# Kernel optimization log

Hardware: AMD Instinct MI355X
Metric: run time of the kernel (lower is better)

Reference implementation:

```python
import jax, jax.numpy as jnp
import numpy as np

N, D, R, DR, H, L = 6000, 128, 1000, 128, 2, 2
MAXN = 1.0 - 4e-3  # Poincare ball projection boundary (c=1)


def _norm(x):
    return jnp.clip(jnp.linalg.norm(x, axis=-1, keepdims=True), 1e-15)


def proj(x):
    n = _norm(x)
    return jnp.where(n > MAXN, x / n * MAXN, x)


def expmap0(u):
    n = _norm(u)
    return proj(jnp.tanh(n) * u / n)


def logmap0(p):
    n = _norm(p)
    return jnp.arctanh(jnp.minimum(n, 1.0 - 1e-7)) * p / n


def mobius_add(x, y):
    x2 = jnp.sum(x * x, -1, keepdims=True)
    y2 = jnp.sum(y * y, -1, keepdims=True)
    xy = jnp.sum(x * y, -1, keepdims=True)
    num = (1 + 2 * xy + y2) * x + (1 - x2) * y
    den = 1 + 2 * xy + x2 * y2
    return num / jnp.clip(den, 1e-15)


def hgc_layer(x, adj, W, b):
    # HypLinear (mobius matvec + hyperbolic bias), HypAgg (tangent-space SpMM), HypAct (relu)
    mv = proj(expmap0(logmap0(x) @ W.T))
    h = proj(mobius_add(mv, proj(expmap0(b))))
    h = proj(expmap0(adj @ logmap0(h)))
    return proj(expmap0(jax.nn.relu(logmap0(h))))


def gat_layer(x, adj, W, a_src, a_dst):
    h = jnp.einsum('nd,hde->hne', x, W)                 # [H,N,D]
    es = jnp.einsum('hne,he->hn', h, a_src)
    ed = jnp.einsum('hne,he->hn', h, a_dst)
    e = jax.nn.leaky_relu(es[:, :, None] + ed[:, None, :], 0.2)  # [H,N,N]
    att = jax.nn.softmax(jnp.where(adj[None] > 0, e, -1e9), axis=-1)
    out = jnp.einsum('hnm,hme->hne', att, h).mean(0)    # head-average -> [N,D]
    return jax.nn.elu(out)


def mha(x, Wq, Wk, Wv, Wfc, g, b):
    # Transformer-style MHA with residual + LayerNorm; x: [N, Lr, D]
    Nn, Lr, _ = x.shape
    split = lambda y: y.reshape(Nn, Lr, H, D).transpose(0, 2, 1, 3)
    q, k, v = split(x @ Wq), split(x @ Wk), split(x @ Wv)
    attn = jax.nn.softmax(jnp.einsum('nhld,nhmd->nhlm', q, k) / jnp.sqrt(jnp.float32(D)), -1)
    o = jnp.einsum('nhlm,nhmd->nhld', attn, v).transpose(0, 2, 1, 3).reshape(Nn, Lr, H * D)
    o = o @ Wfc + x
    mu = o.mean(-1, keepdims=True)
    var = o.var(-1, keepdims=True)
    return g * (o - mu) / jnp.sqrt(var + 1e-6) + b


def _forward(ent_sr, ent_tg, rel_sr, rel_tg, adj_sr, adj_tg, rel_adj_sr, rel_adj_tg,
             gat_W, gat_a_src, gat_a_dst, Wq, Wk, Wv, Wfc, ln_g, ln_b, hgc_W, hgc_b):
    # Relation Aggregator: sparse mm + rowsum normalization
    def rel_agg(radj, remb):
        return (radj @ remb) / radj.sum(-1, keepdims=True)
    sr_rel = rel_agg(rel_adj_sr, rel_sr)
    tg_rel = rel_agg(rel_adj_tg, rel_tg)

    # Attentive Neighbor Aggregator + multi-range fusion (res=True -> range = L+1)
    def branch(x, adj):
        outs, h = [x], x
        for i in range(L):
            h = gat_layer(h, adj, gat_W[i], gat_a_src[i], gat_a_dst[i])
            h = h / jnp.clip(_norm(h), 1e-12)  # F.normalize(dim=1)
            outs.append(h)
        seq = jnp.stack(outs, axis=1)  # [N, L+1, D]
        return mha(seq, Wq, Wk, Wv, Wfc, ln_g, ln_b).mean(1)
    sr = branch(ent_sr, adj_sr)
    tg = branch(ent_tg, adj_tg)

    # Hyperbolic encoder (proj_tan0 is identity for PoincareBall)
    def encode(x, adj):
        h = expmap0(x)
        for i in range(2):
            h = hgc_layer(h, adj, hgc_W[i], hgc_b[i])
        return logmap0(h)
    hs = ent_sr + encode(ent_sr, adj_sr)
    ht = ent_tg + encode(ent_tg, adj_tg)

    return (jnp.concatenate([sr, sr_rel], -1), jnp.concatenate([tg, tg_rel], -1),
            jnp.concatenate([hs, sr_rel], -1), jnp.concatenate([ht, tg_rel], -1))


def setup_inputs() -> dict:
    key = jax.random.key(0)
    ks = jax.random.split(key, 24)

    def make_adj(k):
        m = jax.random.bernoulli(k, 32.0 / N, (N, N)) | jnp.eye(N, dtype=bool)
        a = m.astype(jnp.float32)
        return a / a.sum(-1, keepdims=True)

    def make_rel_adj(k1, k2):
        m = jax.random.bernoulli(k1, 5.0 / R, (N, R)).astype(jnp.float32)
        idx = jax.random.randint(k2, (N,), 0, R)
        return m.at[jnp.arange(N), idx].set(1.0)  # guarantee positive rowsum

    return {
        'ent_sr': 0.02 * jax.random.normal(ks[0], (N, D)),
        'ent_tg': 0.02 * jax.random.normal(ks[1], (N, D)),
        'rel_sr': 0.02 * jax.random.normal(ks[2], (R, DR)),
        'rel_tg': 0.02 * jax.random.normal(ks[3], (R, DR)),
        'adj_sr': make_adj(ks[4]),
        'adj_tg': make_adj(ks[5]),
        'rel_adj_sr': make_rel_adj(ks[6], ks[7]),
        'rel_adj_tg': make_rel_adj(ks[8], ks[9]),
        'gat_W': 0.1 * jax.random.normal(ks[10], (L, H, D, D)),
        'gat_a_src': 0.1 * jax.random.normal(ks[11], (L, H, D)),
        'gat_a_dst': 0.1 * jax.random.normal(ks[12], (L, H, D)),
        'Wq': 0.05 * jax.random.normal(ks[13], (D, H * D)),
        'Wk': 0.05 * jax.random.normal(ks[14], (D, H * D)),
        'Wv': 0.05 * jax.random.normal(ks[15], (D, H * D)),
        'Wfc': 0.05 * jax.random.normal(ks[16], (H * D, D)),
        'ln_g': jnp.ones((D,)),
        'ln_b': jnp.zeros((D,)),
        'hgc_W': 0.05 * jax.random.normal(ks[17], (2, D, D)),
        'hgc_b': 0.01 * jax.random.normal(ks[18], (2, D)),
    }


def reference(ent_sr, ent_tg, rel_sr, rel_tg, adj_sr, adj_tg, rel_adj_sr, rel_adj_tg,
              gat_W, gat_a_src, gat_a_dst, Wq, Wk, Wv, Wfc, ln_g, ln_b, hgc_W, hgc_b):
    return _forward(ent_sr, ent_tg, rel_sr, rel_tg, adj_sr, adj_tg, rel_adj_sr, rel_adj_tg,
                    gat_W, gat_a_src, gat_a_dst, Wq, Wk, Wv, Wfc, ln_g, ln_b, hgc_W, hgc_b)
```

## Files before the change

### kernel.cpp

```cpp
#include <hip/hip_runtime.h>
#include <hip/hip_bf16.h>
#include <math.h>

#define NN   6000
#define N2   12000
#define DD   128
#define RR   1000
#define CAP  96
#define CAPR 48
#define MAXN_F 0.996f

typedef short  bf16x8 __attribute__((ext_vector_type(8)));
typedef float  f32x4  __attribute__((ext_vector_type(4)));
typedef unsigned u32x4 __attribute__((ext_vector_type(4)));

__device__ int      g_dt[19];
__device__ unsigned g_csri[N2 * CAP];
__device__ int      g_cnt[N2];
__device__ float    g_seq[N2 * 3 * DD];
__device__ unsigned short g_seqb[3 * N2 * DD];
__device__ unsigned short g_hhb[N2 * 256];
__device__ float    g_es[2][N2];
__device__ float    g_ed[2][N2];
__device__ unsigned short g_qkvb[(size_t)N2 * 3 * 768];
__device__ unsigned short g_ob[(size_t)N2 * 3 * 256];
__device__ float    g_fc[N2 * 3 * DD];
__device__ float    g_t[N2 * DD];
__device__ float    g_t2[N2 * DD];
__device__ unsigned short g_WgatT[2][256 * DD];
__device__ unsigned short g_WqkvT[768 * DD];
__device__ unsigned short g_WfcT[DD * 256];
__device__ float    g_WhgcT[2][DD * DD];

__device__ __forceinline__ float ldin(const void* p, size_t i, int bf) {
    if (bf) return __uint_as_float(((unsigned)((const unsigned short*)p)[i]) << 16);
    return ((const float*)p)[i];
}
__device__ __forceinline__ unsigned short f2b(float f) {
    unsigned u = __float_as_uint(f);
    u += 0x7FFFu + ((u >> 16) & 1u);
    return (unsigned short)(u >> 16);
}
__device__ __forceinline__ float b2f(unsigned short b) {
    return __uint_as_float(((unsigned)b) << 16);
}
__device__ __forceinline__ float adjval(int c) {
    return b2f(f2b(1.0f / (float)c));
}

__device__ __forceinline__ float wsum(float v) {
    #pragma unroll
    for (int o = 32; o > 0; o >>= 1) v += __shfl_xor(v, o, 64);
    return v;
}
__device__ __forceinline__ float wmax(float v) {
    #pragma unroll
    for (int o = 32; o > 0; o >>= 1) v = fmaxf(v, __shfl_xor(v, o, 64));
    return v;
}

struct P19 { const void* p[19]; };

__global__ void detect_all(P19 ptrs) {
    const int sizes[19] = {768000,768000,128000,128000,36000000,36000000,6000000,6000000,
                           65536,512,512,32768,32768,32768,32768,128,128,32768,256};
    __shared__ int votes[2];
    if (threadIdx.x == 0) { votes[0] = 0; votes[1] = 0; }
    __syncthreads();
    int slot = blockIdx.x < 19 ? blockIdx.x : 17;
    const unsigned* p = (const unsigned*)ptrs.p[slot];
    int nwords = sizes[slot] / 2;
    if (nwords > 0) {
        int nsamp = nwords < 4096 ? nwords : 4096;
        int stride = nwords / nsamp; if (stride < 1) stride = 1;
        for (int s = threadIdx.x; s < nsamp; s += blockDim.x) {
            unsigned lo = p[(size_t)s * stride] & 0xFFFFu;
            if (lo) {
                unsigned e = (lo >> 7) & 0xFFu;
                if (e >= 100u && e <= 140u) atomicAdd(&votes[1], 1);
                else                        atomicAdd(&votes[0], 1);
            }
        }
    }
    __syncthreads();
    int isbf = (votes[1] > votes[0]) ? 1 : 0;
    if (blockIdx.x < 19) {
        if (threadIdx.x == 0) g_dt[blockIdx.x] = isbf;
    } else {
        for (int i = threadIdx.x; i < 32768; i += blockDim.x) {
            int j = i & 127, d = (i >> 7) & 127, l = i >> 14;
            g_WhgcT[l][j * 128 + d] = ldin(ptrs.p[17], i, isbf);
        }
    }
}

__device__ __forceinline__ void bias_wave(const void* hgc_b, int layer, int lane,
                                          float& y0, float& y1, float& y2) {
    float b0 = ldin(hgc_b, (size_t)layer * DD + lane, g_dt[18]);
    float b1 = ldin(hgc_b, (size_t)layer * DD + 64 + lane, g_dt[18]);
    float ss = wsum(b0 * b0 + b1 * b1);
    float nrm = fmaxf(sqrtf(ss), 1e-15f);
    float t = tanhf(nrm);
    float s = t / nrm;
    float vn = t;
    if (t > MAXN_F) { s *= MAXN_F / t; vn = MAXN_F; }
    y0 = s * b0; y1 = s * b1;
    y2 = vn * vn;
}

__device__ __forceinline__ void hgc_lin_w(const float* uw, int layer, int lane,
                                          float y0, float y1, float y2,
                                          float& o0, float& o1) {
    const float* W = g_WhgcT[layer];
    float mv0 = 0.f, mv1 = 0.f;
    #pragma unroll 16
    for (int j = 0; j < DD; j++) {
        float uj = uw[j];
        mv0 = fmaf(W[j * 128 + lane], uj, mv0);
        mv1 = fmaf(W[j * 128 + 64 + lane], uj, mv1);
    }
    float ss2 = wsum(mv0 * mv0 + mv1 * mv1);
    float nm = fmaxf(sqrtf(ss2), 1e-15f);
    float t2 = tanhf(nm);
    float sc = t2 / nm; float xn = t2;
    if (t2 > MAXN_F) { sc *= MAXN_F / t2; xn = MAXN_F; }
    float x0 = sc * mv0, x1 = sc * mv1;
    float x2 = xn * xn;
    float xy = wsum(x0 * y0 + x1 * y1);
    float a = 1.f + 2.f * xy + y2;
    float den = 1.f + 2.f * xy + x2 * y2;
    den = (fabsf(den) < 1e-15f) ? 1e-15f : den;
    float h0 = (a * x0 + (1.f - x2) * y0) / den;
    float h1 = (a * x1 + (1.f - x2) * y1) / den;
    float s3 = wsum(h0 * h0 + h1 * h1);
    float nn = fmaxf(sqrtf(s3), 1e-15f);
    float f = 1.f;
    if (nn > MAXN_F) { f = MAXN_F / nn; nn = MAXN_F; }
    float lg = atanhf(fminf(nn, 1.f - 1e-7f)) / nn;
    o0 = lg * f * h0; o1 = lg * f * h1;
}

__device__ __forceinline__ void hgc_agg_w(const float* tin, int n, int which, int lane,
                                          unsigned* bas, float& o0, float& o1) {
    int c = min(g_cnt[n], CAP);
    const unsigned* idx = &g_csri[(size_t)n * CAP];
    if (lane < c)      bas[lane]      = (idx[lane]      + (unsigned)(which * NN)) * 128u;
    if (64 + lane < c) bas[64 + lane] = (idx[64 + lane] + (unsigned)(which * NN)) * 128u;
    float a0 = 0.f, a1 = 0.f;
    int j = 0;
    for (; j + 4 <= c; j += 4) {
        unsigned b0 = bas[j], b1 = bas[j + 1], b2 = bas[j + 2], b3 = bas[j + 3];
        float v0 = tin[(size_t)b0 + lane], v1 = tin[(size_t)b1 + lane];
        float v2 = tin[(size_t)b2 + lane], v3 = tin[(size_t)b3 + lane];
        float w0 = tin[(size_t)b0 + 64 + lane], w1 = tin[(size_t)b1 + 64 + lane];
        float w2 = tin[(size_t)b2 + 64 + lane], w3 = tin[(size_t)b3 + 64 + lane];
        a0 += (v0 + v1) + (v2 + v3);
        a1 += (w0 + w1) + (w2 + w3);
    }
    for (; j < c; j++) {
        unsigned bb = bas[j];
        a0 += tin[(size_t)bb + lane];
        a1 += tin[(size_t)bb + 64 + lane];
    }
    float sc = (c > 0) ? adjval(c) : 0.f;
    a0 *= sc; a1 *= sc;
    float ss = wsum(a0 * a0 + a1 * a1);
    float nm = fmaxf(sqrtf(ss), 1e-15f);
    float t = tanhf(nm);
    float s1 = t / nm; float xn = t;
    if (t > MAXN_F) { s1 *= MAXN_F / t; xn = MAXN_F; }
    float lg = atanhf(fminf(xn, 1.f - 1e-7f)) / fmaxf(xn, 1e-15f);
    float u0 = fmaxf(lg * s1 * a0, 0.f), u1 = fmaxf(lg * s1 * a1, 0.f);
    float ss2 = wsum(u0 * u0 + u1 * u1);
    float nm2 = fmaxf(sqrtf(ss2), 1e-15f);
    float t2 = tanhf(nm2);
    float s2 = t2 / nm2; float xn2 = t2;
    if (t2 > MAXN_F) { s2 *= MAXN_F / t2; xn2 = MAXN_F; }
    float lg2 = atanhf(fminf(xn2, 1.f - 1e-7f)) / fmaxf(xn2, 1e-15f);
    o0 = lg2 * s2 * u0; o1 = lg2 * s2 * u1;
}

__global__ __launch_bounds__(256) void front_mega(P19 in, float* __restrict__ out) {
    int b = blockIdx.x;
    int tid = threadIdx.x;
    int w = tid >> 6, lane = tid & 63;
    int phase, pb;
    if (b < 9000) { pb = b / 3; phase = b - pb * 3; }
    else { phase = 3; pb = b - 9000; }

    if (phase == 0) {
        int which = pb >= 1500 ? 1 : 0;
        int row = ((which ? pb - 1500 : pb) << 2) | w;
        const void* A = in.p[4 + which];
        int gn = which * NN + row;
        __shared__ int cnt4[4];
        if (lane == 0) cnt4[w] = 0;
        __syncthreads();
        unsigned* dst = &g_csri[(size_t)gn * CAP];
        if (g_dt[4 + which]) {
            const u32x4* p = (const u32x4*)((const unsigned short*)A + (size_t)row * NN);
            #pragma unroll
            for (int c0 = 0; c0 < 12; c0 += 6) {
                u32x4 v[6];
                #pragma unroll
                for (int u = 0; u < 6; u++) {
                    int idx = (c0 + u) * 64 + lane;
                    if (idx < 750) v[u] = __builtin_nontemporal_load(&p[idx]);
                    else v[u] = (u32x4)(0u);
                }
                #pragma unroll
                for (int u = 0; u < 6; u++) {
                    int idx = (c0 + u) * 64 + lane;
                    #pragma unroll
                    for (int h = 0; h < 4; h++) {
                        unsigned w32 = v[u][h];
                        if (w32) {
                            unsigned lo = w32 & 0xFFFFu, hi = w32 >> 16;
                            if (lo && !(lo & 0x8000u)) {
                                int q = atomicAdd(&cnt4[w], 1);
                                if (q < CAP) dst[q] = (unsigned)(idx * 8 + h * 2);
                            }
                            if (hi && !(hi & 0x8000u)) {
                                int q = atomicAdd(&cnt4[w], 1);
                                if (q < CAP) dst[q] = (unsigned)(idx * 8 + h * 2 + 1);
                            }
                        }
                    }
                }
            }
        } else {
            const f32x4* p = (const f32x4*)((const float*)A + (size_t)row * NN);
            #pragma unroll
            for (int c0 = 0; c0 < 24; c0 += 6) {
                f32x4 v[6];
                #pragma unroll
                for (int u = 0; u < 6; u++) {
                    int idx = (c0 + u) * 64 + lane;
                    if (idx < 1500) v[u] = __builtin_nontemporal_load(&p[idx]);
                    else v[u] = (f32x4)(0.f);
                }
                #pragma unroll
                for (int u = 0; u < 6; u++) {
                    int idx = (c0 + u) * 64 + lane;
                    #pragma unroll
                    for (int h = 0; h < 4; h++) {
                        if (v[u][h] > 0.f) {
                            int q = atomicAdd(&cnt4[w], 1);
                            if (q < CAP) dst[q] = (unsigned)(idx * 4 + h);
                        }
                    }
                }
            }
        }
        __syncthreads();
        if (lane == 0) g_cnt[gn] = min(cnt4[w], CAP);
    } else if (phase == 1) {
        int n = pb * 4 + w;
        int which = n >= NN ? 1 : 0;
        int row = n - which * NN;
        const void* radj = in.p[6 + which];
        const void* rel  = in.p[2 + which];
        const int bfa = g_dt[6 + which], bfr = g_dt[2 + which];
        __shared__ int rl_list[4][CAPR];
        __shared__ int rl_cs[4];
        if (lane == 0) rl_cs[w] = 0;
        if (bfa) {
            const uint4* p = (const uint4*)((const unsigned short*)radj + (size_t)row * RR);
            #pragma unroll
            for (int rep = 0; rep < 2; rep++) {
                int i = rep * 64 + lane;
                if (i < 125) {
                    uint4 w4 = p[i];
                    unsigned ws4[4] = {w4.x, w4.y, w4.z, w4.w};
                    #pragma unroll
                    for (int h = 0; h < 4; h++) {
                        unsigned lo = ws4[h] & 0xFFFFu, hi = ws4[h] >> 16;
                        if (lo && !(lo & 0x8000u)) { int q = atomicAdd(&rl_cs[w], 1); if (q < CAPR) rl_list[w][q] = i * 8 + h * 2; }
                        if (hi && !(hi & 0x8000u)) { int q = atomicAdd(&rl_cs[w], 1); if (q < CAPR) rl_list[w][q] = i * 8 + h * 2 + 1; }
                    }
                }
            }
        } else {
            const float4* p = (const float4*)((const float*)radj + (size_t)row * RR);
            #pragma unroll
            for (int rep = 0; rep < 4; rep++) {
                int i = rep * 64 + lane;
                if (i < 250) {
                    float4 w4 = p[i];
                    float vs[4] = {w4.x, w4.y, w4.z, w4.w};
                    #pragma unroll
                    for (int h = 0; h < 4; h++)
                        if (vs[h] > 0.f) { int q = atomicAdd(&rl_cs[w], 1); if (q < CAPR) rl_list[w][q] = i * 4 + h; }
                }
            }
        }
        int c = min(rl_cs[w], CAPR);
        float a0 = 0.f, a1 = 0.f;
        for (int j = 0; j < c; j++) {
            int li = rl_list[w][j];
            a0 += ldin(rel, (size_t)li * DD + lane, bfr);
            a1 += ldin(rel, (size_t)li * DD + 64 + lane, bfr);
        }
        float r0 = c ? a0 / (float)c : 0.f;
        float r1 = c ? a1 / (float)c : 0.f;
        out[(size_t)n * 256 + 128 + lane] = r0;
        out[(size_t)n * 256 + 192 + lane] = r1;
        out[(size_t)(2 * NN + n) * 256 + 128 + lane] = r0;
        out[(size_t)(2 * NN + n) * 256 + 192 + lane] = r1;
    } else if (phase == 2) {
        int n = pb * 4 + w;
        int which = n >= NN ? 1 : 0;
        int row = n - which * NN;
        __shared__ float us[4][128];
        float y0, y1, y2v;
        bias_wave(in.p[18], 0, lane, y0, y1, y2v);
        float x0 = ldin(in.p[which], (size_t)row * DD + lane, g_dt[which]);
        float x1 = ldin(in.p[which], (size_t)row * DD + 64 + lane, g_dt[which]);
        g_seq[(size_t)n * 384 + lane] = x0;
        g_seq[(size_t)n * 384 + 64 + lane] = x1;
        g_seqb[(size_t)n * DD + lane] = f2b(x0);
        g_seqb[(size_t)n * DD + 64 + lane] = f2b(x1);
        float ss = wsum(x0 * x0 + x1 * x1);
        float nrm = fmaxf(sqrtf(ss), 1e-15f);
        float t = tanhf(nrm);
        float scale = t / nrm;
        float hn = t;
        if (t > MAXN_F) { scale *= MAXN_F / t; hn = MAXN_F; }
        float lgx = atanhf(fminf(hn, 1.f - 1e-7f)) / fmaxf(hn, 1e-15f);
        us[w][lane] = lgx * scale * x0;
        us[w][64 + lane] = lgx * scale * x1;
        float o0, o1;
        hgc_lin_w(us[w], 0, lane, y0, y1, y2v, o0, o1);
        g_t[(size_t)n * DD + lane] = o0;
        g_t[(size_t)n * DD + 64 + lane] = o1;
    } else {
        int stride = 128 * 256;
        int base = pb * 256 + tid;
        const int b8 = g_dt[8], b11 = g_dt[11], b12 = g_dt[12], b13 = g_dt[13],
                  b14 = g_dt[14];
        for (int i = base; i < 65536; i += stride) {
            int e = i & 127, d = (i >> 7) & 127, h = (i >> 14) & 1, l = (i >> 15) & 1;
            g_WgatT[l][(h * 128 + e) * DD + d] = f2b(ldin(in.p[8], i, b8));
        }
        for (int i = base; i < 32768; i += stride) {
            int d = i >> 8, e = i & 255;
            g_WqkvT[(size_t)e * DD + d]         = f2b(ldin(in.p[11], i, b11));
            g_WqkvT[(size_t)(256 + e) * DD + d] = f2b(ldin(in.p[12], i, b12));
            g_WqkvT[(size_t)(512 + e) * DD + d] = f2b(ldin(in.p[13], i, b13));
        }
        for (int i = base; i < 32768; i += stride) {
            int e = i >> 7, dd = i & 127;
            g_WfcT[dd * 256 + e] = f2b(ldin(in.p[14], i, b14));
        }
    }
}

__global__ __launch_bounds__(256) void gemm_scores(P19 in, int layer) {
    int tid = threadIdx.x;
    int w = tid >> 6, lane = tid & 63;
    int q = lane >> 4, ln = lane & 15;
    int bm = blockIdx.x * 16;
    const unsigned short* A = g_seqb + (size_t)layer * (N2 * DD);
    const unsigned short* Bt = g_WgatT[layer];
    int colbase = w * 64;
    f32x4 acc[4] = {};
    #pragma unroll
    for (int s = 0; s < 4; s++) {
        int kc = s * 4 + q;
        bf16x8 af = *(const bf16x8*)(A + (size_t)(bm + ln) * DD + kc * 8);
        #pragma unroll
        for (int nt = 0; nt < 4; nt++) {
            bf16x8 bf = *(const bf16x8*)(Bt + (size_t)(colbase + nt * 16 + ln) * DD + kc * 8);
            acc[nt] = __builtin_amdgcn_mfma_f32_16x16x32_bf16(af, bf, acc[nt], 0, 0, 0);
        }
    }
    #pragma unroll
    for (int nt = 0; nt < 4; nt++) {
        int col = colbase + nt * 16 + ln;
        #pragma unroll
        for (int r = 0; r < 4; r++) {
            int row = bm + q * 4 + r;
            g_hhb[(size_t)row * 256 + col] = f2b(acc[nt][r]);
        }
    }
    const int bfs = g_dt[9], bfd = g_dt[10];
    float a_s[4], a_d[4];
    #pragma unroll
    for (int nt = 0; nt < 4; nt++) {
        int col = colbase + nt * 16 + ln;
        size_t ab = ((size_t)layer * 2 + (col >> 7)) * DD + (col & 127);
        a_s[nt] = ldin(in.p[9],  ab, bfs);
        a_d[nt] = ldin(in.p[10], ab, bfd);
    }
    __shared__ float pS[4][16], pD[4][16];
    #pragma unroll
    for (int r = 0; r < 4; r++) {
        float ps = 0.f, pd = 0.f;
        #pragma unroll
        for (int nt = 0; nt < 4; nt++) {
            ps = fmaf(acc[nt][r], a_s[nt], ps);
            pd = fmaf(acc[nt][r], a_d[nt], pd);
        }
        #pragma unroll
        for (int o = 1; o < 16; o <<= 1) {
            ps += __shfl_xor(ps, o, 64);
            pd += __shfl_xor(pd, o, 64);
        }
        if (ln == 0) { pS[w][q * 4 + r] = ps; pD[w][q * 4 + r] = pd; }
    }
    __syncthreads();
    if (tid < 16) {
        g_es[0][bm + tid] = pS[0][tid] + pS[1][tid];
        g_es[1][bm + tid] = pS[2][tid] + pS[3][tid];
        g_ed[0][bm + tid] = pD[0][tid] + pD[1][tid];
        g_ed[1][bm + tid] = pD[2][tid] + pD[3][tid];
    }
}

__global__ __launch_bounds__(256) void gemm_qkv() {
    __shared__ __align__(16) unsigned short As[16 * 128 * 8];
    __shared__ __align__(16) unsigned short Bs[16 * 128 * 8];
    int bm = blockIdx.y * 128, bn = blockIdx.x * 128;
    int tid = threadIdx.x;
    int lane = tid & 63, w = tid >> 6;
    int q = lane >> 4, ln = lane & 15;
    const int M = N2 * 3;
    f32x4 acc[8][2] = {};
    #pragma unroll
    for (int i = 0; i < 8; i++) {
        int combo = w * 8 + i;
        int c = combo >> 1, half = combo & 1;
        int r = half * 64 + lane;
        int gm = bm + r; if (gm >= M) gm = M - 1;
        int n = gm / 3, l = gm - n * 3;
        *(uint4*)&As[(c * 128 + r) * 8] =
            *(const uint4*)(g_seqb + (size_t)l * (N2 * DD) + (size_t)n * DD + c * 8);
        *(uint4*)&Bs[(c * 128 + r) * 8] =
            *(const uint4*)(g_WqkvT + (size_t)(bn + r) * DD + c * 8);
    }
    __syncthreads();
    #pragma unroll
    for (int s = 0; s < 4; s++) {
        bf16x8 bf0 = *(const bf16x8*)&Bs[((s * 4 + q) * 128 + w * 32 + ln) * 8];
        bf16x8 bf1 = *(const bf16x8*)&Bs[((s * 4 + q) * 128 + w * 32 + 16 + ln) * 8];
        #pragma unroll
        for (int mt = 0; mt < 8; mt++) {
            bf16x8 af = *(const bf16x8*)&As[((s * 4 + q) * 128 + mt * 16 + ln) * 8];
            acc[mt][0] = __builtin_amdgcn_mfma_f32_16x16x32_bf16(af, bf0, acc[mt][0], 0, 0, 0);
            acc[mt][1] = __builtin_amdgcn_mfma_f32_16x16x32_bf16(af, bf1, acc[mt][1], 0, 0, 0);
        }
    }
    #pragma unroll
    for (int mt = 0; mt < 8; mt++) {
        #pragma unroll
        for (int nt = 0; nt < 2; nt++) {
            int gcol = bn + w * 32 + nt * 16 + ln;
            #pragma unroll
            for (int r = 0; r < 4; r++) {
                int grow = bm + mt * 16 + q * 4 + r;
                if (grow < M)
                    g_qkvb[(size_t)grow * 768 + gcol] = f2b(acc[mt][nt][r]);
            }
        }
    }
}

__global__ __launch_bounds__(256) void gemm_fc() {
    __shared__ __align__(16) unsigned short As[16 * 128 * 8];
    __shared__ __align__(16) unsigned short Bs[16 * 128 * 8];
    int bm = blockIdx.x * 128;
    int tid = threadIdx.x;
    int lane = tid & 63, w = tid >> 6;
    int q = lane >> 4, ln = lane & 15;
    const int M = N2 * 3;
    f32x4 acc[8][2] = {};
    for (int k0 = 0; k0 < 256; k0 += 128) {
        if (k0 > 0) __syncthreads();
        #pragma unroll
        for (int i = 0; i < 8; i++) {
            int combo = w * 8 + i;
            int c = combo >> 1, half = combo & 1;
            int r = half * 64 + lane;
            int gm = bm + r; if (gm >= M) gm = M - 1;
            *(uint4*)&As[(c * 128 + r) * 8] =
                *(const uint4*)(g_ob + (size_t)gm * 256 + k0 + c * 8);
            *(uint4*)&Bs[(c * 128 + r) * 8] =
                *(const uint4*)(g_WfcT + (size_t)r * 256 + k0 + c * 8);
        }
        __syncthreads();
        #pragma unroll
        for (int s = 0; s < 4; s++) {
            bf16x8 bf0 = *(const bf16x8*)&Bs[((s * 4 + q) * 128 + w * 32 + ln) * 8];
            bf16x8 bf1 = *(const bf16x8*)&Bs[((s * 4 + q) * 128 + w * 32 + 16 + ln) * 8];
            #pragma unroll
            for (int mt = 0; mt < 8; mt++) {
                bf16x8 af = *(const bf16x8*)&As[((s * 4 + q) * 128 + mt * 16 + ln) * 8];
                acc[mt][0] = __builtin_amdgcn_mfma_f32_16x16x32_bf16(af, bf0, acc[mt][0], 0, 0, 0);
                acc[mt][1] = __builtin_amdgcn_mfma_f32_16x16x32_bf16(af, bf1, acc[mt][1], 0, 0, 0);
            }
        }
    }
    #pragma unroll
    for (int mt = 0; mt < 8; mt++) {
        #pragma unroll
        for (int nt = 0; nt < 2; nt++) {
            int gcol = w * 32 + nt * 16 + ln;
            #pragma unroll
            for (int r = 0; r < 4; r++) {
                int grow = bm + mt * 16 + q * 4 + r;
                if (grow < M)
                    g_fc[(size_t)grow * 128 + gcol] = acc[mt][nt][r];
            }
        }
    }
}

__global__ __launch_bounds__(256) void gat_attn(int layer) {
    int tid = threadIdx.x;
    int w = tid >> 6, lane = tid & 63;
    int n = blockIdx.x * 4 + w;
    int which = n >= NN ? 1 : 0;
    int c = min(g_cnt[n], CAP);
    __shared__ unsigned bas[4][CAP];
    __shared__ float w0s[4][CAP], w1s[4][CAP];
    float es0 = g_es[0][n], es1 = g_es[1][n];
    float e0a = -1e30f, e1a = -1e30f, e0b = -1e30f, e1b = -1e30f;
    if (lane < c) {
        int gI = (int)g_csri[(size_t)n * CAP + lane] + which * NN;
        bas[w][lane] = (unsigned)gI * 128u;
        e0a = es0 + g_ed[0][gI]; e0a = e0a > 0.f ? e0a : 0.2f * e0a;
        e1a = es1 + g_ed[1][gI]; e1a = e1a > 0.f ? e1a : 0.2f * e1a;
    }
    if (64 + lane < c) {
        int gI = (int)g_csri[(size_t)n * CAP + 64 + lane] + which * NN;
        bas[w][64 + lane] = (unsigned)gI * 128u;
        e0b = es0 + g_ed[0][gI]; e0b = e0b > 0.f ? e0b : 0.2f * e0b;
        e1b = es1 + g_ed[1][gI]; e1b = e1b > 0.f ? e1b : 0.2f * e1b;
    }
    float m0 = wmax(fmaxf(e0a, e0b));
    float m1 = wmax(fmaxf(e1a, e1b));
    float x0a = (lane < c) ? expf(e0a - m0) : 0.f;
    float x1a = (lane < c) ? expf(e1a - m1) : 0.f;
    float x0b = (64 + lane < c) ? expf(e0b - m0) : 0.f;
    float x1b = (64 + lane < c) ? expf(e1b - m1) : 0.f;
    float s0 = wsum(x0a + x0b), s1 = wsum(x1a + x1b);
    float r0 = 1.f / fmaxf(s0, 1e-30f), r1 = 1.f / fmaxf(s1, 1e-30f);
    if (lane < c)      { w0s[w][lane] = x0a * r0;      w1s[w][lane] = x1a * r1; }
    if (64 + lane < c) { w0s[w][64 + lane] = x0b * r0; w1s[w][64 + lane] = x1b * r1; }
    const unsigned* hh32 = (const unsigned*)g_hhb;
    float aLe = 0.f, aLo = 0.f, aHe = 0.f, aHo = 0.f;
    #pragma unroll 4
    for (int j = 0; j < c; j++) {
        unsigned bb = bas[w][j];
        unsigned vlo = hh32[(size_t)bb + lane];
        unsigned vhi = hh32[(size_t)bb + 64 + lane];
        float g0 = w0s[w][j], g1 = w1s[w][j];
        aLe = fmaf(g0, b2f((unsigned short)(vlo & 0xFFFFu)), aLe);
        aLo = fmaf(g0, b2f((unsigned short)(vlo >> 16)), aLo);
        aHe = fmaf(g1, b2f((unsigned short)(vhi & 0xFFFFu)), aHe);
        aHo = fmaf(g1, b2f((unsigned short)(vhi >> 16)), aHo);
    }
    float o0 = (c > 0) ? 0.5f * (aLe + aHe) : 0.f;
    float o1 = (c > 0) ? 0.5f * (aLo + aHo) : 0.f;
    o0 = o0 > 0.f ? o0 : expm1f(o0);
    o1 = o1 > 0.f ? o1 : expm1f(o1);
    float ss = wsum(o0 * o0 + o1 * o1);
    float rn = 1.f / fmaxf(sqrtf(ss), 1e-12f);
    o0 *= rn; o1 *= rn;
    g_seq[(size_t)n * 384 + (layer + 1) * 128 + 2 * lane] = o0;
    g_seq[(size_t)n * 384 + (layer + 1) * 128 + 2 * lane + 1] = o1;
    size_t pbase = (size_t)(layer + 1) * (N2 * DD) + (size_t)n * DD + 2 * lane;
    *(unsigned*)&g_seqb[pbase] = (unsigned)f2b(o0) | ((unsigned)f2b(o1) << 16);
}

__global__ __launch_bounds__(256) void attn_mid(const void* __restrict__ hgc_b) {
    int tid = threadIdx.x;
    int w = tid >> 6, lane = tid & 63;
    if (blockIdx.x < 3000) {
        int n = blockIdx.x * 4 + w;
        int d0 = lane * 4;
        const unsigned short* row = g_qkvb + (size_t)n * 2304;
        float qf[3][4], kf[3][4], vf[3][4];
        #pragma unroll
        for (int l = 0; l < 3; l++) {
            uint2 qv = *(const uint2*)(row + l * 768 + d0);
            uint2 kv = *(const uint2*)(row + l * 768 + 256 + d0);
            uint2 vv = *(const uint2*)(row + l * 768 + 512 + d0);
            qf[l][0] = b2f((unsigned short)(qv.x & 0xFFFFu)); qf[l][1] = b2f((unsigned short)(qv.x >> 16));
            qf[l][2] = b2f((unsigned short)(qv.y & 0xFFFFu)); qf[l][3] = b2f((unsigned short)(qv.y >> 16));
            kf[l][0] = b2f((unsigned short)(kv.x & 0xFFFFu)); kf[l][1] = b2f((unsigned short)(kv.x >> 16));
            kf[l][2] = b2f((unsigned short)(kv.y & 0xFFFFu)); kf[l][3] = b2f((unsigned short)(kv.y >> 16));
            vf[l][0] = b2f((unsigned short)(vv.x & 0xFFFFu)); vf[l][1] = b2f((unsigned short)(vv.x >> 16));
            vf[l][2] = b2f((unsigned short)(vv.y & 0xFFFFu)); vf[l][3] = b2f((unsigned short)(vv.y >> 16));
        }
        float att[3][3];
        #pragma unroll
        for (int l = 0; l < 3; l++) {
            #pragma unroll
            for (int m = 0; m < 3; m++) {
                float p = 0.f;
                #pragma unroll
                for (int i = 0; i < 4; i++) p = fmaf(qf[l][i], kf[m][i], p);
                #pragma unroll
                for (int o = 16; o > 0; o >>= 1) p += __shfl_xor(p, o, 64);
                att[l][m] = p * 0.08838834764831845f;
            }
        }
        #pragma unroll
        for (int l = 0; l < 3; l++) {
            float mx = fmaxf(att[l][0], fmaxf(att[l][1], att[l][2]));
            float e0 = expf(att[l][0] - mx), e1 = expf(att[l][1] - mx), e2 = expf(att[l][2] - mx);
            float s = 1.f / fmaxf(e0 + e1 + e2, 1e-30f);
            att[l][0] = e0 * s; att[l][1] = e1 * s; att[l][2] = e2 * s;
        }
        unsigned short* orow = g_ob + (size_t)n * 768;
        #pragma unroll
        for (int l = 0; l < 3; l++) {
            float o[4];
            #pragma unroll
            for (int i = 0; i < 4; i++)
                o[i] = att[l][0] * vf[0][i] + att[l][1] * vf[1][i] + att[l][2] * vf[2][i];
            uint2 pk;
            pk.x = (unsigned)f2b(o[0]) | ((unsigned)f2b(o[1]) << 16);
            pk.y = (unsigned)f2b(o[2]) | ((unsigned)f2b(o[3]) << 16);
            *(uint2*)(orow + l * 256 + d0) = pk;
        }
    } else {
        int n = (blockIdx.x - 3000) * 4 + w;
        int which = n >= NN ? 1 : 0;
        __shared__ unsigned bas[4][CAP];
        __shared__ float us[4][128];
        float y0, y1, y2v;
        bias_wave(hgc_b, 1, lane, y0, y1, y2v);
        float u0, u1;
        hgc_agg_w(g_t, n, which, lane, bas[w], u0, u1);
        us[w][lane] = u0; us[w][64 + lane] = u1;
        float o0, o1;
        hgc_lin_w(us[w], 1, lane, y0, y1, y2v, o0, o1);
        g_t2[(size_t)n * DD + lane] = o0;
        g_t2[(size_t)n * DD + 64 + lane] = o1;
    }
}

__global__ __launch_bounds__(256) void out_fin(const void* __restrict__ g, const void* __restrict__ b,
                                               const void* __restrict__ e0, const void* __restrict__ e1,
                                               float* __restrict__ out) {
    int tid = threadIdx.x;
    int w = tid >> 6, lane = tid & 63;
    if (blockIdx.x < 3000) {
        int n = blockIdx.x * 4 + w;
        const int bg = g_dt[15], bb = g_dt[16];
        float ool0[3], ool1[3], mu[3], rstd[3];
        #pragma unroll
        for (int l = 0; l < 3; l++) {
            ool0[l] = g_fc[(size_t)(n * 3 + l) * 128 + lane] + g_seq[(size_t)(n * 3 + l) * 128 + lane];
            ool1[l] = g_fc[(size_t)(n * 3 + l) * 128 + 64 + lane] + g_seq[(size_t)(n * 3 + l) * 128 + 64 + lane];
        }
        #pragma unroll
        for (int l = 0; l < 3; l++) {
            float s  = wsum(ool0[l] + ool1[l]);
            float ss = wsum(ool0[l] * ool0[l] + ool1[l] * ool1[l]);
            mu[l] = s / 128.f;
            rstd[l] = rsqrtf(ss / 128.f - mu[l] * mu[l] + 1e-6f);
        }
        float acc0 = 0.f, acc1 = 0.f;
        #pragma unroll
        for (int l = 0; l < 3; l++) {
            acc0 += (ool0[l] - mu[l]) * rstd[l];
            acc1 += (ool1[l] - mu[l]) * rstd[l];
        }
        out[(size_t)n * 256 + lane]      = ldin(g, lane, bg) * (acc0 / 3.f) + ldin(b, lane, bb);
        out[(size_t)n * 256 + 64 + lane] = ldin(g, 64 + lane, bg) * (acc1 / 3.f) + ldin(b, 64 + lane, bb);
    } else {
        int n = (blockIdx.x - 3000) * 4 + w;
        int which = n >= NN ? 1 : 0;
        __shared__ unsigned bas[4][CAP];
        float u0, u1;
        hgc_agg_w(g_t2, n, which, lane, bas[w], u0, u1);
        float ev0 = ldin(which ? e1 : e0, (size_t)(n - which * NN) * DD + lane, g_dt[which]);
        float ev1 = ldin(which ? e1 : e0, (size_t)(n - which * NN) * DD + 64 + lane, g_dt[which]);
        out[(size_t)(2 * NN + n) * 256 + lane]      = ev0 + u0;
        out[(size_t)(2 * NN + n) * 256 + 64 + lane] = ev1 + u1;
    }
}

extern "C" void kernel_launch(void* const* d_in, const int* in_sizes, int n_in,
                              void* d_out, int out_size, void* d_ws, size_t ws_size,
                              hipStream_t stream) {
    const void* ln_g = d_in[15];
    const void* ln_b = d_in[16];
    const void* hgc_b = d_in[18];

    float* out = (float*)d_out;

    P19 ptrs;
    for (int i = 0; i < 19; i++) ptrs.p[i] = d_in[i];
    detect_all<<<20, 1024, 0, stream>>>(ptrs);

    front_mega<<<9128, 256, 0, stream>>>(ptrs, out);

    gemm_scores<<<750, 256, 0, stream>>>(ptrs, 0);
    gat_attn<<<3000, 256, 0, stream>>>(0);
    gemm_scores<<<750, 256, 0, stream>>>(ptrs, 1);
    gat_attn<<<3000, 256, 0, stream>>>(1);

    gemm_qkv<<<dim3(6, 282), 256, 0, stream>>>();
    attn_mid<<<6000, 256, 0, stream>>>(hgc_b);
    gemm_fc<<<282, 256, 0, stream>>>();
    out_fin<<<6000, 256, 0, stream>>>(ln_g, ln_b, d_in[0], d_in[1], out);
}
```

Measured before the change: 595.8 us.

## Fold Wq·Wk and Wv·Wfc into fused weights to drop FC GEMM

Precomputes per-head products Wq_h·Wk_h^T and Wv_h·Wfc_h as a 512-column fused weight, so one GEMM produces Z (query projected into key space) and Y (value already through the FC). Attention scores are then dot products of Z with the raw input, and the output is an attention-weighted sum of Y. The FC GEMM and its fp32 intermediate go away, and LayerNorm moves into the middle kernel, which removes one launch and the qkv/o/fc buffers. The weight products are computed in the detect kernel with scalar loops, which adds setup work, and rounding the fused weights to bf16 changes numerical error.

```diff
diff --git a/kernel.cpp b/kernel.cpp
--- a/kernel.cpp
+++ b/kernel.cpp
@@ -22,14 +22,11 @@
 __device__ unsigned short g_hhb[N2 * 256];
 __device__ float    g_es[2][N2];
 __device__ float    g_ed[2][N2];
-__device__ unsigned short g_qkvb[(size_t)N2 * 3 * 768];
-__device__ unsigned short g_ob[(size_t)N2 * 3 * 256];
-__device__ float    g_fc[N2 * 3 * DD];
+__device__ unsigned short g_zy[(size_t)N2 * 3 * 512];
 __device__ float    g_t[N2 * DD];
 __device__ float    g_t2[N2 * DD];
 __device__ unsigned short g_WgatT[2][256 * DD];
-__device__ unsigned short g_WqkvT[768 * DD];
-__device__ unsigned short g_WfcT[DD * 256];
+__device__ unsigned short g_WzyT[512 * DD];
 __device__ float    g_WhgcT[2][DD * DD];
 
 __device__ __forceinline__ float ldin(const void* p, size_t i, int bf) {
@@ -61,35 +58,72 @@
 
 struct P19 { const void* p[19]; };
 
+__device__ __forceinline__ int vote_bf(const unsigned* p, int nwords, int tid, int nthr,
+                                       int* votes) {
+    int nsamp = nwords < 2048 ? nwords : 2048;
+    int stride = nwords / nsamp; if (stride < 1) stride = 1;
+    for (int s = tid; s < nsamp; s += nthr) {
+        unsigned lo = p[(size_t)s * stride] & 0xFFFFu;
+        if (lo) {
+            unsigned e = (lo >> 7) & 0xFFu;
+            if (e >= 100u && e <= 140u) atomicAdd(&votes[1], 1);
+            else                        atomicAdd(&votes[0], 1);
+        }
+    }
+    __syncthreads();
+    return votes[1] > votes[0] ? 1 : 0;
+}
+
 __global__ void detect_all(P19 ptrs) {
     const int sizes[19] = {768000,768000,128000,128000,36000000,36000000,6000000,6000000,
                            65536,512,512,32768,32768,32768,32768,128,128,32768,256};
     __shared__ int votes[2];
-    if (threadIdx.x == 0) { votes[0] = 0; votes[1] = 0; }
-    __syncthreads();
-    int slot = blockIdx.x < 19 ? blockIdx.x : 17;
-    const unsigned* p = (const unsigned*)ptrs.p[slot];
-    int nwords = sizes[slot] / 2;
-    if (nwords > 0) {
-        int nsamp = nwords < 4096 ? nwords : 4096;
-        int stride = nwords / nsamp; if (stride < 1) stride = 1;
-        for (int s = threadIdx.x; s < nsamp; s += blockDim.x) {
-            unsigned lo = p[(size_t)s * stride] & 0xFFFFu;
-            if (lo) {
-                unsigned e = (lo >> 7) & 0xFFu;
-                if (e >= 100u && e <= 140u) atomicAdd(&votes[1], 1);
-                else                        atomicAdd(&votes[0], 1);
-            }
-        }
-    }
-    __syncthreads();
-    int isbf = (votes[1] > votes[0]) ? 1 : 0;
-    if (blockIdx.x < 19) {
-        if (threadIdx.x == 0) g_dt[blockIdx.x] = isbf;
+    int tid = threadIdx.x;
+    if (blockIdx.x < 20) {
+        if (tid == 0) { votes[0] = 0; votes[1] = 0; }
+        __syncthreads();
+        int slot = blockIdx.x < 19 ? blockIdx.x : 17;
+        int isbf = vote_bf((const unsigned*)ptrs.p[slot], sizes[slot] / 2, tid, blockDim.x, votes);
+        if (blockIdx.x < 19) {
+            if (tid == 0) g_dt[blockIdx.x] = isbf;
+        } else {
+            for (int i = tid; i < 32768; i += blockDim.x) {
+                int j = i & 127, d = (i >> 7) & 127, l = i >> 14;
+                g_WhgcT[l][j * 128 + d] = ldin(ptrs.p[17], i, isbf);
+            }
+        }
     } else {
-        for (int i = threadIdx.x; i < 32768; i += blockDim.x) {
-            int j = i & 127, d = (i >> 7) & 127, l = i >> 14;
-            g_WhgcT[l][j * 128 + d] = ldin(ptrs.p[17], i, isbf);
+        int pi = blockIdx.x - 20;
+        int matsel = pi >> 2;
+        int slotA = matsel ? 13 : 11;
+        int slotB = matsel ? 14 : 12;
+        if (tid == 0) { votes[0] = 0; votes[1] = 0; }
+        __syncthreads();
+        int bfA = vote_bf((const unsigned*)ptrs.p[slotA], 16384, tid, blockDim.x, votes);
+        __syncthreads();
+        if (tid == 0) { votes[0] = 0; votes[1] = 0; }
+        __syncthreads();
+        int bfB = vote_bf((const unsigned*)ptrs.p[slotB], 16384, tid, blockDim.x, votes);
+        const void* A = ptrs.p[slotA];
+        const void* B = ptrs.p[slotB];
+        int c0 = matsel * 256 + (pi & 3) * 64;
+        for (int t = tid; t < 64 * 128; t += blockDim.x) {
+            int cl = t >> 7, i = t & 127;
+            int c = c0 + cl;
+            int h = (c >> 7) & 1, oo = c & 127;
+            float acc = 0.f;
+            if (matsel == 0) {
+                #pragma unroll 8
+                for (int e = 0; e < 128; e++)
+                    acc = fmaf(ldin(A, (size_t)i * 256 + h * 128 + e, bfA),
+                               ldin(B, (size_t)oo * 256 + h * 128 + e, bfB), acc);
+            } else {
+                #pragma unroll 8
+                for (int e = 0; e < 128; e++)
+                    acc = fmaf(ldin(A, (size_t)i * 256 + h * 128 + e, bfA),
+                               ldin(B, (size_t)(h * 128 + e) * 128 + oo, bfB), acc);
+            }
+            g_WzyT[(size_t)c * 128 + i] = f2b(acc);
         }
     }
 }
@@ -336,21 +370,10 @@
     } else {
         int stride = 128 * 256;
         int base = pb * 256 + tid;
-        const int b8 = g_dt[8], b11 = g_dt[11], b12 = g_dt[12], b13 = g_dt[13],
-                  b14 = g_dt[14];
+        const int b8 = g_dt[8];
         for (int i = base; i < 65536; i += stride) {
             int e = i & 127, d = (i >> 7) & 127, h = (i >> 14) & 1, l = (i >> 15) & 1;
             g_WgatT[l][(h * 128 + e) * DD + d] = f2b(ldin(in.p[8], i, b8));
-        }
-        for (int i = base; i < 32768; i += stride) {
-            int d = i >> 8, e = i & 255;
-            g_WqkvT[(size_t)e * DD + d]         = f2b(ldin(in.p[11], i, b11));
-            g_WqkvT[(size_t)(256 + e) * DD + d] = f2b(ldin(in.p[12], i, b12));
-            g_WqkvT[(size_t)(512 + e) * DD + d] = f2b(ldin(in.p[13], i, b13));
-        }
-        for (int i = base; i < 32768; i += stride) {
-            int e = i >> 7, dd = i & 127;
-            g_WfcT[dd * 256 + e] = f2b(ldin(in.p[14], i, b14));
         }
     }
 }
@@ -417,7 +440,7 @@
     }
 }
 
-__global__ __launch_bounds__(256) void gemm_qkv() {
+__global__ __launch_bounds__(256) void gemm_zy() {
     __shared__ __align__(16) unsigned short As[16 * 128 * 8];
     __shared__ __align__(16) unsigned short Bs[16 * 128 * 8];
     int bm = blockIdx.y * 128, bn = blockIdx.x * 128;
@@ -436,7 +459,7 @@
         *(uint4*)&As[(c * 128 + r) * 8] =
             *(const uint4*)(g_seqb + (size_t)l * (N2 * DD) + (size_t)n * DD + c * 8);
         *(uint4*)&Bs[(c * 128 + r) * 8] =
-            *(const uint4*)(g_WqkvT + (size_t)(bn + r) * DD + c * 8);
+            *(const uint4*)(g_WzyT + (size_t)(bn + r) * DD + c * 8);
     }
     __syncthreads();
     #pragma unroll
@@ -459,57 +482,7 @@
             for (int r = 0; r < 4; r++) {
                 int grow = bm + mt * 16 + q * 4 + r;
                 if (grow < M)
-                    g_qkvb[(size_t)grow * 768 + gcol] = f2b(acc[mt][nt][r]);
-            }
-        }
-    }
-}
-
-__global__ __launch_bounds__(256) void gemm_fc() {
-    __shared__ __align__(16) unsigned short As[16 * 128 * 8];
-    __shared__ __align__(16) unsigned short Bs[16 * 128 * 8];
-    int bm = blockIdx.x * 128;
-    int tid = threadIdx.x;
-    int lane = tid & 63, w = tid >> 6;
-    int q = lane >> 4, ln = lane & 15;
-    const int M = N2 * 3;
-    f32x4 acc[8][2] = {};
-    for (int k0 = 0; k0 < 256; k0 += 128) {
-        if (k0 > 0) __syncthreads();
-        #pragma unroll
-        for (int i = 0; i < 8; i++) {
-            int combo = w * 8 + i;
-            int c = combo >> 1, half = combo & 1;
-            int r = half * 64 + lane;
-            int gm = bm + r; if (gm >= M) gm = M - 1;
-            *(uint4*)&As[(c * 128 + r) * 8] =
-                *(const uint4*)(g_ob + (size_t)gm * 256 + k0 + c * 8);
-            *(uint4*)&Bs[(c * 128 + r) * 8] =
-                *(const uint4*)(g_WfcT + (size_t)r * 256 + k0 + c * 8);
-        }
-        __syncthreads();
-        #pragma unroll
-        for (int s = 0; s < 4; s++) {
-            bf16x8 bf0 = *(const bf16x8*)&Bs[((s * 4 + q) * 128 + w * 32 + ln) * 8];
-            bf16x8 bf1 = *(const bf16x8*)&Bs[((s * 4 + q) * 128 + w * 32 + 16 + ln) * 8];
-            #pragma unroll
-            for (int mt = 0; mt < 8; mt++) {
-                bf16x8 af = *(const bf16x8*)&As[((s * 4 + q) * 128 + mt * 16 + ln) * 8];
-                acc[mt][0] = __builtin_amdgcn_mfma_f32_16x16x32_bf16(af, bf0, acc[mt][0], 0, 0, 0);
-                acc[mt][1] = __builtin_amdgcn_mfma_f32_16x16x32_bf16(af, bf1, acc[mt][1], 0, 0, 0);
-            }
-        }
-    }
-    #pragma unroll
-    for (int mt = 0; mt < 8; mt++) {
-        #pragma unroll
-        for (int nt = 0; nt < 2; nt++) {
-            int gcol = w * 32 + nt * 16 + ln;
-            #pragma unroll
-            for (int r = 0; r < 4; r++) {
-                int grow = bm + mt * 16 + q * 4 + r;
-                if (grow < M)
-                    g_fc[(size_t)grow * 128 + gcol] = acc[mt][nt][r];
+                    g_zy[(size_t)grow * 512 + gcol] = f2b(acc[mt][nt][r]);
             }
         }
     }
@@ -573,58 +546,93 @@
     *(unsigned*)&g_seqb[pbase] = (unsigned)f2b(o0) | ((unsigned)f2b(o1) << 16);
 }
 
-__global__ __launch_bounds__(256) void attn_mid(const void* __restrict__ hgc_b) {
+__global__ __launch_bounds__(256) void mha_mid(const void* __restrict__ hgc_b,
+                                               const void* __restrict__ g,
+                                               const void* __restrict__ bb_,
+                                               float* __restrict__ out) {
     int tid = threadIdx.x;
     int w = tid >> 6, lane = tid & 63;
     if (blockIdx.x < 3000) {
         int n = blockIdx.x * 4 + w;
-        int d0 = lane * 4;
-        const unsigned short* row = g_qkvb + (size_t)n * 2304;
-        float qf[3][4], kf[3][4], vf[3][4];
+        int dl = 2 * lane;
+        float xm[3][2], zf[3][2][2];
         #pragma unroll
         for (int l = 0; l < 3; l++) {
-            uint2 qv = *(const uint2*)(row + l * 768 + d0);
-            uint2 kv = *(const uint2*)(row + l * 768 + 256 + d0);
-            uint2 vv = *(const uint2*)(row + l * 768 + 512 + d0);
-            qf[l][0] = b2f((unsigned short)(qv.x & 0xFFFFu)); qf[l][1] = b2f((unsigned short)(qv.x >> 16));
-            qf[l][2] = b2f((unsigned short)(qv.y & 0xFFFFu)); qf[l][3] = b2f((unsigned short)(qv.y >> 16));
-            kf[l][0] = b2f((unsigned short)(kv.x & 0xFFFFu)); kf[l][1] = b2f((unsigned short)(kv.x >> 16));
-            kf[l][2] = b2f((unsigned short)(kv.y & 0xFFFFu)); kf[l][3] = b2f((unsigned short)(kv.y >> 16));
-            vf[l][0] = b2f((unsigned short)(vv.x & 0xFFFFu)); vf[l][1] = b2f((unsigned short)(vv.x >> 16));
-            vf[l][2] = b2f((unsigned short)(vv.y & 0xFFFFu)); vf[l][3] = b2f((unsigned short)(vv.y >> 16));
-        }
-        float att[3][3];
+            unsigned xv = *(const unsigned*)(g_seqb + (size_t)l * (N2 * DD) + (size_t)n * DD + dl);
+            xm[l][0] = b2f((unsigned short)(xv & 0xFFFFu));
+            xm[l][1] = b2f((unsigned short)(xv >> 16));
+            size_t zb = (size_t)(n * 3 + l) * 512;
+            #pragma unroll
+            for (int h = 0; h < 2; h++) {
+                unsigned zv = *(const unsigned*)(g_zy + zb + h * 128 + dl);
+                zf[l][h][0] = b2f((unsigned short)(zv & 0xFFFFu));
+                zf[l][h][1] = b2f((unsigned short)(zv >> 16));
+            }
+        }
+        float att[2][3][3];
+        #pragma unroll
+        for (int h = 0; h < 2; h++)
+            #pragma unroll
+            for (int l = 0; l < 3; l++)
+                #pragma unroll
+                for (int m = 0; m < 3; m++) {
+                    float p = zf[l][h][0] * xm[m][0] + zf[l][h][1] * xm[m][1];
+                    #pragma unroll
+                    for (int o = 32; o > 0; o >>= 1) p += __shfl_xor(p, o, 64);
+                    att[h][l][m] = p * 0.08838834764831845f;
+                }
+        #pragma unroll
+        for (int h = 0; h < 2; h++)
+            #pragma unroll
+            for (int l = 0; l < 3; l++) {
+                float mx = fmaxf(att[h][l][0], fmaxf(att[h][l][1], att[h][l][2]));
+                float ea = expf(att[h][l][0] - mx), eb = expf(att[h][l][1] - mx),
+                      ec = expf(att[h][l][2] - mx);
+                float s = 1.f / fmaxf(ea + eb + ec, 1e-30f);
+                att[h][l][0] = ea * s; att[h][l][1] = eb * s; att[h][l][2] = ec * s;
+            }
+        float yv[3][2][2];
+        #pragma unroll
+        for (int m = 0; m < 3; m++) {
+            size_t yb = (size_t)(n * 3 + m) * 512 + 256;
+            #pragma unroll
+            for (int h = 0; h < 2; h++) {
+                unsigned v = *(const unsigned*)(g_zy + yb + h * 128 + dl);
+                yv[m][h][0] = b2f((unsigned short)(v & 0xFFFFu));
+                yv[m][h][1] = b2f((unsigned short)(v >> 16));
+            }
+        }
+        float ool[3][2], mu[3], rstd[3];
         #pragma unroll
         for (int l = 0; l < 3; l++) {
-            #pragma unroll
-            for (int m = 0; m < 3; m++) {
-                float p = 0.f;
+            float f0 = 0.f, f1 = 0.f;
+            #pragma unroll
+            for (int h = 0; h < 2; h++)
                 #pragma unroll
-                for (int i = 0; i < 4; i++) p = fmaf(qf[l][i], kf[m][i], p);
-                #pragma unroll
-                for (int o = 16; o > 0; o >>= 1) p += __shfl_xor(p, o, 64);
-                att[l][m] = p * 0.08838834764831845f;
-            }
+                for (int m = 0; m < 3; m++) {
+                    f0 = fmaf(att[h][l][m], yv[m][h][0], f0);
+                    f1 = fmaf(att[h][l][m], yv[m][h][1], f1);
+                }
+            const float* sq = g_seq + (size_t)n * 384 + l * 128 + dl;
+            ool[l][0] = f0 + sq[0];
+            ool[l][1] = f1 + sq[1];
         }
         #pragma unroll
         for (int l = 0; l < 3; l++) {
-            float mx = fmaxf(att[l][0], fmaxf(att[l][1], att[l][2]));
-            float e0 = expf(att[l][0] - mx), e1 = expf(att[l][1] - mx), e2 = expf(att[l][2] - mx);
-            float s = 1.f / fmaxf(e0 + e1 + e2, 1e-30f);
-            att[l][0] = e0 * s; att[l][1] = e1 * s; att[l][2] = e2 * s;
-        }
-        unsigned short* orow = g_ob + (size_t)n * 768;
+            float s  = wsum(ool[l][0] + ool[l][1]);
+            float ss = wsum(ool[l][0] * ool[l][0] + ool[l][1] * ool[l][1]);
+            mu[l] = s / 128.f;
+            rstd[l] = rsqrtf(ss / 128.f - mu[l] * mu[l] + 1e-6f);
+        }
+        float acc0 = 0.f, acc1 = 0.f;
         #pragma unroll
         for (int l = 0; l < 3; l++) {
-            float o[4];
-            #pragma unroll
-            for (int i = 0; i < 4; i++)
-                o[i] = att[l][0] * vf[0][i] + att[l][1] * vf[1][i] + att[l][2] * vf[2][i];
-            uint2 pk;
-            pk.x = (unsigned)f2b(o[0]) | ((unsigned)f2b(o[1]) << 16);
-            pk.y = (unsigned)f2b(o[2]) | ((unsigned)f2b(o[3]) << 16);
-            *(uint2*)(orow + l * 256 + d0) = pk;
-        }
+            acc0 += (ool[l][0] - mu[l]) * rstd[l];
+            acc1 += (ool[l][1] - mu[l]) * rstd[l];
+        }
+        const int bg = g_dt[15], bb = g_dt[16];
+        out[(size_t)n * 256 + dl]     = ldin(g, dl, bg) * (acc0 / 3.f) + ldin(bb_, dl, bb);
+        out[(size_t)n * 256 + dl + 1] = ldin(g, dl + 1, bg) * (acc1 / 3.f) + ldin(bb_, dl + 1, bb);
     } else {
         int n = (blockIdx.x - 3000) * 4 + w;
         int which = n >= NN ? 1 : 0;
@@ -642,46 +650,20 @@
     }
 }
 
-__global__ __launch_bounds__(256) void out_fin(const void* __restrict__ g, const void* __restrict__ b,
-                                               const void* __restrict__ e0, const void* __restrict__ e1,
+__global__ __launch_bounds__(256) void hgc_fin(const void* __restrict__ e0,
+                                               const void* __restrict__ e1,
                                                float* __restrict__ out) {
     int tid = threadIdx.x;
     int w = tid >> 6, lane = tid & 63;
-    if (blockIdx.x < 3000) {
-        int n = blockIdx.x * 4 + w;
-        const int bg = g_dt[15], bb = g_dt[16];
-        float ool0[3], ool1[3], mu[3], rstd[3];
-        #pragma unroll
-        for (int l = 0; l < 3; l++) {
-            ool0[l] = g_fc[(size_t)(n * 3 + l) * 128 + lane] + g_seq[(size_t)(n * 3 + l) * 128 + lane];
-            ool1[l] = g_fc[(size_t)(n * 3 + l) * 128 + 64 + lane] + g_seq[(size_t)(n * 3 + l) * 128 + 64 + lane];
-        }
-        #pragma unroll
-        for (int l = 0; l < 3; l++) {
-            float s  = wsum(ool0[l] + ool1[l]);
-            float ss = wsum(ool0[l] * ool0[l] + ool1[l] * ool1[l]);
-            mu[l] = s / 128.f;
-            rstd[l] = rsqrtf(ss / 128.f - mu[l] * mu[l] + 1e-6f);
-        }
-        float acc0 = 0.f, acc1 = 0.f;
-        #pragma unroll
-        for (int l = 0; l < 3; l++) {
-            acc0 += (ool0[l] - mu[l]) * rstd[l];
-            acc1 += (ool1[l] - mu[l]) * rstd[l];
-        }
-        out[(size_t)n * 256 + lane]      = ldin(g, lane, bg) * (acc0 / 3.f) + ldin(b, lane, bb);
-        out[(size_t)n * 256 + 64 + lane] = ldin(g, 64 + lane, bg) * (acc1 / 3.f) + ldin(b, 64 + lane, bb);
-    } else {
-        int n = (blockIdx.x - 3000) * 4 + w;
-        int which = n >= NN ? 1 : 0;
-        __shared__ unsigned bas[4][CAP];
-        float u0, u1;
-        hgc_agg_w(g_t2, n, which, lane, bas[w], u0, u1);
-        float ev0 = ldin(which ? e1 : e0, (size_t)(n - which * NN) * DD + lane, g_dt[which]);
-        float ev1 = ldin(which ? e1 : e0, (size_t)(n - which * NN) * DD + 64 + lane, g_dt[which]);
-        out[(size_t)(2 * NN + n) * 256 + lane]      = ev0 + u0;
-        out[(size_t)(2 * NN + n) * 256 + 64 + lane] = ev1 + u1;
-    }
+    int n = blockIdx.x * 4 + w;
+    int which = n >= NN ? 1 : 0;
+    __shared__ unsigned bas[4][CAP];
+    float u0, u1;
+    hgc_agg_w(g_t2, n, which, lane, bas[w], u0, u1);
+    float ev0 = ldin(which ? e1 : e0, (size_t)(n - which * NN) * DD + lane, g_dt[which]);
+    float ev1 = ldin(which ? e1 : e0, (size_t)(n - which * NN) * DD + 64 + lane, g_dt[which]);
+    out[(size_t)(2 * NN + n) * 256 + lane]      = ev0 + u0;
+    out[(size_t)(2 * NN + n) * 256 + 64 + lane] = ev1 + u1;
 }
 
 extern "C" void kernel_launch(void* const* d_in, const int* in_sizes, int n_in,
@@ -695,7 +677,7 @@
 
     P19 ptrs;
     for (int i = 0; i < 19; i++) ptrs.p[i] = d_in[i];
-    detect_all<<<20, 1024, 0, stream>>>(ptrs);
+    detect_all<<<28, 1024, 0, stream>>>(ptrs);
 
     front_mega<<<9128, 256, 0, stream>>>(ptrs, out);
 
@@ -704,8 +686,7 @@
     gemm_scores<<<750, 256, 0, stream>>>(ptrs, 1);
     gat_attn<<<3000, 256, 0, stream>>>(1);
 
-    gemm_qkv<<<dim3(6, 282), 256, 0, stream>>>();
-    attn_mid<<<6000, 256, 0, stream>>>(hgc_b);
-    gemm_fc<<<282, 256, 0, stream>>>();
-    out_fin<<<6000, 256, 0, stream>>>(ln_g, ln_b, d_in[0], d_in[1], out);
-}
+    gemm_zy<<<dim3(4, 282), 256, 0, stream>>>();
+    mha_mid<<<6000, 256, 0, stream>>>(hgc_b, ln_g, ln_b, out);
+    hgc_fin<<<3000, 256, 0, stream>>>(d_in[0], d_in[1], out);
+}
```

Result: slower. 1.048 ms (+75.9%).
